# Kernel optimization log

Hardware: AMD Instinct MI355X
Metric: run time of the kernel (lower is better)

## Reference

```python
import jax, jax.numpy as jnp
import numpy as np

N, IN_FEAT, OUT_FEAT, H = 4096, 256, 256, 8
D = OUT_FEAT // H  # per-head dim = 32
ADJ_DENSITY = 0.05


def setup_inputs() -> dict:
    key = jax.random.key(0)
    kx, kw, kb, ka, kadj = jax.random.split(key, 5)
    x = jax.random.normal(kx, (N, IN_FEAT), dtype=jnp.float32)
    # eqx.nn.Linear params: weight [out, in], bias [out]
    W = jax.random.normal(kw, (OUT_FEAT, IN_FEAT), dtype=jnp.float32) * (1.0 / np.sqrt(IN_FEAT))
    b = jax.random.normal(kb, (OUT_FEAT,), dtype=jnp.float32) * 0.01
    a = jax.random.normal(ka, (H, 2 * D), dtype=jnp.float32)
    adj_matrix = jax.random.bernoulli(kadj, ADJ_DENSITY, (N, N)).astype(jnp.float32)
    return {"x": x, "W": W, "b": b, "a": a, "adj_matrix": adj_matrix}


def reference(x, W, b, a, adj_matrix):
    num_nodes = x.shape[0]
    num_heads = a.shape[0]
    half = a.shape[1] // 2
    # projection: [N, H*D] -> [N, H, D]
    node_feats = (x @ W.T + b).reshape(num_nodes, num_heads, half)
    # per-head additive attention halves -> [N, H]
    logit_parent = (node_feats * a[None, :, :half]).sum(axis=-1)
    logit_child = (node_feats * a[None, :, half:]).sum(axis=-1)
    # [N, N, H] dense logits via broadcast-add
    attn_logits = logit_parent[:, None, :] + logit_child[None, :, :]
    attn_logits = jax.nn.leaky_relu(attn_logits, 0.2)
    # NOTE: faithful to source — masked entries set to 0.0 (not -inf)
    attn_logits = jnp.where(jnp.abs(adj_matrix)[..., None] != 0.0, attn_logits, 0.0)
    attn_probs = jax.nn.softmax(attn_logits, axis=1)
    out = jnp.einsum('ijh,jhc->ihc', attn_probs, node_feats)
    return out.reshape(num_nodes, -1)
```

## Files before the change

kernel.cpp:

```cpp
#include <hip/hip_runtime.h>

#define NN    4096
#define OF    256
#define NH    8
#define MAXNZ 384

typedef __attribute__((ext_vector_type(8))) short short8;
typedef __attribute__((ext_vector_type(4))) float f32x4;

__device__ __forceinline__ float bf2f(unsigned int u) {
    union { unsigned int i; float f; } v; v.i = u << 16; return v.f;
}
__device__ __forceinline__ unsigned short f2bf(float f) {
    union { float f; unsigned int i; } v; v.f = f;
    unsigned int x = v.i;
    return (unsigned short)((x + 0x7fffu + ((x >> 16) & 1u)) >> 16);
}
__device__ __forceinline__ unsigned int pk2bf(float a, float b) {
    return (unsigned int)f2bf(a) | ((unsigned int)f2bf(b) << 16);
}

__global__ __launch_bounds__(256) void k_proj(
    const void* __restrict__ xraw, const void* __restrict__ Wraw,
    const void* __restrict__ braw, const void* __restrict__ araw,
    const float* __restrict__ adjf,
    unsigned short* __restrict__ nfb, float* __restrict__ lp,
    float* __restrict__ lc, float* __restrict__ Stot, int* __restrict__ flag,
    unsigned short* __restrict__ csr, int* __restrict__ nnz)
{
    __shared__ int viol;
    int t = threadIdx.x;
    if (t == 0) viol = 0;
    __syncthreads();
    int bad = 0;
    for (int k = t; k < NN; k += 256) {
        float v = adjf[k];
        if (!(v == 0.0f || v == 1.0f)) bad = 1;
    }
    if (bad) atomicAdd(&viol, 1);
    __syncthreads();
    int f = viol > 0;
    if (t == 0 && blockIdx.x == 0) *flag = f;

    int wave = t >> 6;
    int lane = t & 63;
    int tid  = blockIdx.x * 4 + wave;
    int mt = tid >> 4, nt = tid & 15;
    int lr = lane & 15;
    int kq = (lane >> 4) * 8;

    f32x4 acc = {0.f, 0.f, 0.f, 0.f};
    if (f) {
        const short8* xp = reinterpret_cast<const short8*>(
            (const unsigned short*)xraw + (size_t)(mt*16 + lr)*OF + kq);
        const short8* wp = reinterpret_cast<const short8*>(
            (const unsigned short*)Wraw + (size_t)(nt*16 + lr)*OF + kq);
        #pragma unroll
        for (int kk = 0; kk < OF/32; kk++)
            acc = __builtin_amdgcn_mfma_f32_16x16x32_bf16(xp[kk*4], wp[kk*4], acc, 0, 0, 0);
    } else {
        const float* xp = (const float*)xraw + (size_t)(mt*16 + lr)*OF + kq;
        const float* wp = (const float*)Wraw + (size_t)(nt*16 + lr)*OF + kq;
        #pragma unroll
        for (int kk = 0; kk < OF/32; kk++) {
            short8 ah, al, bh, bl;
            #pragma unroll
            for (int e = 0; e < 8; e++) {
                float xv = xp[kk*32 + e];
                unsigned short h = f2bf(xv);
                ah[e] = (short)h; al[e] = (short)f2bf(xv - bf2f(h));
                float wv = wp[kk*32 + e];
                unsigned short g = f2bf(wv);
                bh[e] = (short)g; bl[e] = (short)f2bf(wv - bf2f(g));
            }
            acc = __builtin_amdgcn_mfma_f32_16x16x32_bf16(ah, bh, acc, 0, 0, 0);
            acc = __builtin_amdgcn_mfma_f32_16x16x32_bf16(ah, bl, acc, 0, 0, 0);
            acc = __builtin_amdgcn_mfma_f32_16x16x32_bf16(al, bh, acc, 0, 0, 0);
        }
    }

    int col  = nt*16 + lr;
    int row0 = mt*16 + (lane >> 4) * 4;
    int h = col >> 5, cc = col & 31;
    float bias, apar, achd;
    if (f) {
        bias = bf2f((unsigned int)((const unsigned short*)braw)[col]);
        apar = bf2f((unsigned int)((const unsigned short*)araw)[h*64 + cc]);
        achd = bf2f((unsigned int)((const unsigned short*)araw)[h*64 + 32 + cc]);
    } else {
        bias = ((const float*)braw)[col];
        apar = ((const float*)araw)[h*64 + cc];
        achd = ((const float*)araw)[h*64 + 32 + cc];
    }
    float st = 0.f, pr[4], cr[4];
    #pragma unroll
    for (int r = 0; r < 4; r++) {
        float v = acc[r] + bias;
        nfb[(size_t)(row0 + r) * OF + col] = f2bf(v);
        st += v;
        pr[r] = v * apar;
        cr[r] = v * achd;
    }
    #pragma unroll
    for (int m = 1; m <= 8; m <<= 1) {
        #pragma unroll
        for (int r = 0; r < 4; r++) {
            pr[r] += __shfl_xor(pr[r], m, 64);
            cr[r] += __shfl_xor(cr[r], m, 64);
        }
    }
    if ((lane & 15) == 0) {
        #pragma unroll
        for (int r = 0; r < 4; r++) {
            atomicAdd(&lp[(row0 + r) * NH + h], pr[r]);
            atomicAdd(&lc[(row0 + r) * NH + h], cr[r]);
        }
    }
    st += __shfl_down(st, 16, 64);
    st += __shfl_down(st, 32, 64);
    if (lane < 16) atomicAdd(&Stot[col], st);

    int r = tid;
    unsigned long long m64 = 0ULL;
    if (f) {
        const uint4* arow = reinterpret_cast<const uint4*>(
            (const unsigned short*)adjf + (size_t)r * NN);
        #pragma unroll
        for (int g = 0; g < 8; g++) {
            uint4 v = arow[lane + 64*g];
            unsigned int wd[4] = {v.x, v.y, v.z, v.w};
            #pragma unroll
            for (int u = 0; u < 4; u++) {
                if (wd[u] & 0xffffu) m64 |= 1ULL << (g*8 + 2*u);
                if (wd[u] >> 16)     m64 |= 1ULL << (g*8 + 2*u + 1);
            }
        }
    } else {
        const uint4* arow = reinterpret_cast<const uint4*>(adjf + (size_t)r * NN);
        #pragma unroll 8
        for (int g = 0; g < 16; g++) {
            uint4 v = arow[lane + 64*g];
            if (v.x) m64 |= 1ULL << (g*4);
            if (v.y) m64 |= 1ULL << (g*4 + 1);
            if (v.z) m64 |= 1ULL << (g*4 + 2);
            if (v.w) m64 |= 1ULL << (g*4 + 3);
        }
    }
    int pc = __popcll(m64);
    int pref = pc;
    #pragma unroll
    for (int off = 1; off < 64; off <<= 1) {
        int u = __shfl_up(pref, off, 64);
        if (lane >= off) pref += u;
    }
    if (lane == 63) nnz[r] = min(pref, MAXNZ);
    {
        int pos = pref - pc;
        unsigned long long mm = m64;
        while (mm && pos < MAXNZ) {
            int q = __builtin_ctzll(mm);
            mm &= mm - 1;
            int j = f ? (lane*8 + ((q >> 3) << 9) + (q & 7))
                      : (lane*4 + ((q >> 2) << 8) + (q & 3));
            csr[(size_t)r * MAXNZ + pos++] = (unsigned short)j;
        }
    }
}

__global__ __launch_bounds__(256, 8) void k_attn(
    const int* __restrict__ flag, const unsigned short* __restrict__ csr,
    const int* __restrict__ nnz,
    const float* __restrict__ lp, const float* __restrict__ lc,
    const unsigned short* __restrict__ nfb, const float* __restrict__ Stot,
    void* __restrict__ outv)
{
    __shared__ float lps[NH];
    __shared__ int   jro[MAXNZ];
    __shared__ float wlist[MAXNZ][NH];
    __shared__ float zred[256];
    __shared__ float gred[3][256];

    int i = blockIdx.x;
    int t = threadIdx.x;
    int lane = t & 63, wid = t >> 6;
    int f = *flag;
    if (t < NH) lps[t] = lp[i*NH + t];
    int n = min(nnz[i], MAXNZ);

    if (t < MAXNZ/8) {
        uint4 v = reinterpret_cast<const uint4*>(csr + (size_t)i * MAXNZ)[t];
        unsigned int ws[4] = {v.x, v.y, v.z, v.w};
        #pragma unroll
        for (int u = 0; u < 4; u++) {
            jro[t*8 + 2*u]     = (int)(ws[u] & 0xffffu) * OF;
            jro[t*8 + 2*u + 1] = (int)(ws[u] >> 16) * OF;
        }
    }
    __syncthreads();

    int h8 = t & 7, c32 = t >> 3;
    float lph = lps[h8];
    float zp = 0.f;
    int k3 = c32;
    for (; k3 + 32 < n; k3 += 64) {
        int j0 = jro[k3] >> 5, j1 = jro[k3 + 32] >> 5;
        float l0 = lc[j0 + h8], l1 = lc[j1 + h8];
        float s0 = lph + l0; s0 = s0 > 0.f ? s0 : 0.2f * s0;
        float s1 = lph + l1; s1 = s1 > 0.f ? s1 : 0.2f * s1;
        float w0 = __expf(fminf(s0, 70.f)) - 1.f;
        float w1 = __expf(fminf(s1, 70.f)) - 1.f;
        wlist[k3][h8] = w0; wlist[k3 + 32][h8] = w1;
        zp += w0 + w1;
    }
    if (k3 < n) {
        float s = lph + lc[(jro[k3] >> 5) + h8];
        s = s > 0.f ? s : 0.2f * s;
        float w = __expf(fminf(s, 70.f)) - 1.f;
        wlist[k3][h8] = w;
        zp += w;
    }
    zred[t] = zp;
    __syncthreads();

    int hh = lane >> 3;
    int c4 = lane * 4;
    float a0 = 0.f, a1 = 0.f, a2 = 0.f, a3 = 0.f;
    int k = wid;
    for (; k + 28 < n; k += 32) {
        int jj[8]; float ww[8];
        #pragma unroll
        for (int u = 0; u < 8; u++) {
            jj[u] = __builtin_amdgcn_readfirstlane(jro[k + 4*u]);
            ww[u] = wlist[k + 4*u][hh];
        }
        uint2 d[8];
        #pragma unroll
        for (int u = 0; u < 8; u++)
            d[u] = *reinterpret_cast<const uint2*>(nfb + jj[u] + c4);
        #pragma unroll
        for (int u = 0; u < 8; u++) {
            a0 += ww[u] * bf2f(d[u].x & 0xffffu);
            a1 += ww[u] * bf2f(d[u].x >> 16);
            a2 += ww[u] * bf2f(d[u].y & 0xffffu);
            a3 += ww[u] * bf2f(d[u].y >> 16);
        }
    }
    for (; k < n; k += 4) {
        int j = __builtin_amdgcn_readfirstlane(jro[k]);
        float w = wlist[k][hh];
        uint2 d = *reinterpret_cast<const uint2*>(nfb + j + c4);
        a0 += w * bf2f(d.x & 0xffffu);
        a1 += w * bf2f(d.x >> 16);
        a2 += w * bf2f(d.y & 0xffffu);
        a3 += w * bf2f(d.y >> 16);
    }
    if (wid) {
        gred[wid-1][c4]   = a0; gred[wid-1][c4+1] = a1;
        gred[wid-1][c4+2] = a2; gred[wid-1][c4+3] = a3;
    }
    __syncthreads();

    if (wid == 0) {
        float z = zred[lane] + zred[lane+64] + zred[lane+128] + zred[lane+192];
        z += __shfl_down(z, 32, 64);
        z += __shfl_down(z, 16, 64);
        z += __shfl_down(z, 8, 64);
        float zfull = __shfl(z, hh, 64);
        float iz = 1.0f / (4096.0f + zfull);
        a0 += gred[0][c4]   + gred[1][c4]   + gred[2][c4];
        a1 += gred[0][c4+1] + gred[1][c4+1] + gred[2][c4+1];
        a2 += gred[0][c4+2] + gred[1][c4+2] + gred[2][c4+2];
        a3 += gred[0][c4+3] + gred[1][c4+3] + gred[2][c4+3];
        float4 stv = *reinterpret_cast<const float4*>(Stot + c4);
        float o0 = (stv.x + a0) * iz;
        float o1 = (stv.y + a1) * iz;
        float o2 = (stv.z + a2) * iz;
        float o3 = (stv.w + a3) * iz;
        if (f) {
            uint2 pk; pk.x = pk2bf(o0, o1); pk.y = pk2bf(o2, o3);
            *reinterpret_cast<uint2*>((unsigned short*)outv + (size_t)i*OF + c4) = pk;
        } else {
            float4 o = {o0, o1, o2, o3};
            *reinterpret_cast<float4*>((float*)outv + (size_t)i*OF + c4) = o;
        }
    }
}

extern "C" void kernel_launch(void* const* d_in, const int* in_sizes, int n_in,
                              void* d_out, int out_size, void* d_ws, size_t ws_size,
                              hipStream_t stream) {
    const void* x   = d_in[0];
    const void* W   = d_in[1];
    const void* b   = d_in[2];
    const void* a   = d_in[3];
    const void* adj = d_in[4];

    char* ws = (char*)d_ws;
    const size_t MB = 1024u*1024u, KB = 1024u;
    unsigned short* nfb  = (unsigned short*)(ws);
    float*          lp   = (float*)(ws + 2*MB);
    float*          lc   = (float*)(ws + 2*MB + 128*KB);
    float*          Stot = (float*)(ws + 2*MB + 256*KB);
    int*            flag = (int*)(ws + 2*MB + 257*KB);
    unsigned short* csr  = (unsigned short*)(ws + 2*MB + 258*KB);
    int*            nnz  = (int*)(ws + 5*MB + 258*KB);

    hipMemsetAsync(lp, 0, 257*KB, stream);
    k_proj <<<1024, 256, 0, stream>>>(x, W, b, a, (const float*)adj,
                                      nfb, lp, lc, Stot, flag, csr, nnz);
    k_attn <<<NN,   256, 0, stream>>>(flag, csr, nnz, lp, lc, nfb, Stot, d_out);
}
```

Before: 156.5 us.

## Split preprocessing kernel: precompute bf16 hi/lo splits of x and W

Adds a k_pre kernel that does the adjacency-to-CSR compaction and, on the fp32 path, converts x and W once into bf16 high/low halves stored in workspace. k_proj then loads these pre-split short8 vectors directly instead of doing strided scalar fp32 loads and per-element conversion inside every MFMA tile, where each W element was converted redundantly by many waves. In exchange it adds an extra kernel launch, writes and reads about 8 MB of extra workspace traffic, and reads the flag from global memory.

```diff
diff --git a/kernel.cpp b/kernel.cpp
--- a/kernel.cpp
+++ b/kernel.cpp
@@ -20,13 +20,12 @@
     return (unsigned int)f2bf(a) | ((unsigned int)f2bf(b) << 16);
 }
 
-__global__ __launch_bounds__(256) void k_proj(
-    const void* __restrict__ xraw, const void* __restrict__ Wraw,
-    const void* __restrict__ braw, const void* __restrict__ araw,
-    const float* __restrict__ adjf,
-    unsigned short* __restrict__ nfb, float* __restrict__ lp,
-    float* __restrict__ lc, float* __restrict__ Stot, int* __restrict__ flag,
-    unsigned short* __restrict__ csr, int* __restrict__ nnz)
+__global__ __launch_bounds__(256) void k_pre(
+    const float* __restrict__ adjf, const float* __restrict__ xf,
+    const float* __restrict__ Wf, int* __restrict__ flag,
+    unsigned short* __restrict__ csr, int* __restrict__ nnz,
+    unsigned short* __restrict__ xbh, unsigned short* __restrict__ xbl,
+    unsigned short* __restrict__ Wbh, unsigned short* __restrict__ Wbl)
 {
     __shared__ int viol;
     int t = threadIdx.x;
@@ -42,6 +41,81 @@
     int f = viol > 0;
     if (t == 0 && blockIdx.x == 0) *flag = f;
 
+    int lane = t & 63, wid = t >> 6;
+    int r = blockIdx.x * 4 + wid;
+
+    unsigned long long m64 = 0ULL;
+    if (f) {
+        const uint4* arow = reinterpret_cast<const uint4*>(
+            (const unsigned short*)adjf + (size_t)r * NN);
+        #pragma unroll
+        for (int g = 0; g < 8; g++) {
+            uint4 v = arow[lane + 64*g];
+            unsigned int wd[4] = {v.x, v.y, v.z, v.w};
+            #pragma unroll
+            for (int u = 0; u < 4; u++) {
+                if (wd[u] & 0xffffu) m64 |= 1ULL << (g*8 + 2*u);
+                if (wd[u] >> 16)     m64 |= 1ULL << (g*8 + 2*u + 1);
+            }
+        }
+    } else {
+        const uint4* arow = reinterpret_cast<const uint4*>(adjf + (size_t)r * NN);
+        #pragma unroll 8
+        for (int g = 0; g < 16; g++) {
+            uint4 v = arow[lane + 64*g];
+            if (v.x) m64 |= 1ULL << (g*4);
+            if (v.y) m64 |= 1ULL << (g*4 + 1);
+            if (v.z) m64 |= 1ULL << (g*4 + 2);
+            if (v.w) m64 |= 1ULL << (g*4 + 3);
+        }
+    }
+    int pc = __popcll(m64);
+    int pref = pc;
+    #pragma unroll
+    for (int off = 1; off < 64; off <<= 1) {
+        int u = __shfl_up(pref, off, 64);
+        if (lane >= off) pref += u;
+    }
+    if (lane == 63) nnz[r] = min(pref, MAXNZ);
+    {
+        int pos = pref - pc;
+        unsigned long long mm = m64;
+        while (mm && pos < MAXNZ) {
+            int q = __builtin_ctzll(mm);
+            mm &= mm - 1;
+            int j = f ? (lane*8 + ((q >> 3) << 9) + (q & 7))
+                      : (lane*4 + ((q >> 2) << 8) + (q & 3));
+            csr[(size_t)r * MAXNZ + pos++] = (unsigned short)j;
+        }
+    }
+
+    if (!f) {
+        const int NX = NN * OF, NTOT = NX + OF * OF;
+        for (int e = blockIdx.x * 256 + t; e < NTOT; e += 1024 * 256) {
+            if (e < NX) {
+                float v = xf[e];
+                unsigned short h = f2bf(v);
+                xbh[e] = h; xbl[e] = f2bf(v - bf2f(h));
+            } else {
+                float v = Wf[e - NX];
+                unsigned short h = f2bf(v);
+                Wbh[e - NX] = h; Wbl[e - NX] = f2bf(v - bf2f(h));
+            }
+        }
+    }
+}
+
+__global__ __launch_bounds__(256) void k_proj(
+    const void* __restrict__ xraw, const void* __restrict__ Wraw,
+    const void* __restrict__ braw, const void* __restrict__ araw,
+    const int* __restrict__ flag,
+    const unsigned short* __restrict__ xbh, const unsigned short* __restrict__ xbl,
+    const unsigned short* __restrict__ Wbh, const unsigned short* __restrict__ Wbl,
+    unsigned short* __restrict__ nfb, float* __restrict__ lp,
+    float* __restrict__ lc, float* __restrict__ Stot)
+{
+    int f = *flag;
+    int t = threadIdx.x;
     int wave = t >> 6;
     int lane = t & 63;
     int tid  = blockIdx.x * 4 + wave;
@@ -49,30 +123,25 @@
     int lr = lane & 15;
     int kq = (lane >> 4) * 8;
 
+    size_t xo = (size_t)(mt*16 + lr)*OF + kq;
+    size_t wo = (size_t)(nt*16 + lr)*OF + kq;
+
     f32x4 acc = {0.f, 0.f, 0.f, 0.f};
     if (f) {
-        const short8* xp = reinterpret_cast<const short8*>(
-            (const unsigned short*)xraw + (size_t)(mt*16 + lr)*OF + kq);
-        const short8* wp = reinterpret_cast<const short8*>(
-            (const unsigned short*)Wraw + (size_t)(nt*16 + lr)*OF + kq);
+        const short8* xp = reinterpret_cast<const short8*>((const unsigned short*)xraw + xo);
+        const short8* wp = reinterpret_cast<const short8*>((const unsigned short*)Wraw + wo);
         #pragma unroll
         for (int kk = 0; kk < OF/32; kk++)
             acc = __builtin_amdgcn_mfma_f32_16x16x32_bf16(xp[kk*4], wp[kk*4], acc, 0, 0, 0);
     } else {
-        const float* xp = (const float*)xraw + (size_t)(mt*16 + lr)*OF + kq;
-        const float* wp = (const float*)Wraw + (size_t)(nt*16 + lr)*OF + kq;
+        const short8* xh = reinterpret_cast<const short8*>(xbh + xo);
+        const short8* xl = reinterpret_cast<const short8*>(xbl + xo);
+        const short8* wh = reinterpret_cast<const short8*>(Wbh + wo);
+        const short8* wl = reinterpret_cast<const short8*>(Wbl + wo);
         #pragma unroll
         for (int kk = 0; kk < OF/32; kk++) {
-            short8 ah, al, bh, bl;
-            #pragma unroll
-            for (int e = 0; e < 8; e++) {
-                float xv = xp[kk*32 + e];
-                unsigned short h = f2bf(xv);
-                ah[e] = (short)h; al[e] = (short)f2bf(xv - bf2f(h));
-                float wv = wp[kk*32 + e];
-                unsigned short g = f2bf(wv);
-                bh[e] = (short)g; bl[e] = (short)f2bf(wv - bf2f(g));
-            }
+            short8 ah = xh[kk*4], al = xl[kk*4];
+            short8 bh = wh[kk*4], bl = wl[kk*4];
             acc = __builtin_amdgcn_mfma_f32_16x16x32_bf16(ah, bh, acc, 0, 0, 0);
             acc = __builtin_amdgcn_mfma_f32_16x16x32_bf16(ah, bl, acc, 0, 0, 0);
             acc = __builtin_amdgcn_mfma_f32_16x16x32_bf16(al, bh, acc, 0, 0, 0);
@@ -119,52 +188,6 @@
     st += __shfl_down(st, 16, 64);
     st += __shfl_down(st, 32, 64);
     if (lane < 16) atomicAdd(&Stot[col], st);
-
-    int r = tid;
-    unsigned long long m64 = 0ULL;
-    if (f) {
-        const uint4* arow = reinterpret_cast<const uint4*>(
-            (const unsigned short*)adjf + (size_t)r * NN);
-        #pragma unroll
-        for (int g = 0; g < 8; g++) {
-            uint4 v = arow[lane + 64*g];
-            unsigned int wd[4] = {v.x, v.y, v.z, v.w};
-            #pragma unroll
-            for (int u = 0; u < 4; u++) {
-                if (wd[u] & 0xffffu) m64 |= 1ULL << (g*8 + 2*u);
-                if (wd[u] >> 16)     m64 |= 1ULL << (g*8 + 2*u + 1);
-            }
-        }
-    } else {
-        const uint4* arow = reinterpret_cast<const uint4*>(adjf + (size_t)r * NN);
-        #pragma unroll 8
-        for (int g = 0; g < 16; g++) {
-            uint4 v = arow[lane + 64*g];
-            if (v.x) m64 |= 1ULL << (g*4);
-            if (v.y) m64 |= 1ULL << (g*4 + 1);
-            if (v.z) m64 |= 1ULL << (g*4 + 2);
-            if (v.w) m64 |= 1ULL << (g*4 + 3);
-        }
-    }
-    int pc = __popcll(m64);
-    int pref = pc;
-    #pragma unroll
-    for (int off = 1; off < 64; off <<= 1) {
-        int u = __shfl_up(pref, off, 64);
-        if (lane >= off) pref += u;
-    }
-    if (lane == 63) nnz[r] = min(pref, MAXNZ);
-    {
-        int pos = pref - pc;
-        unsigned long long mm = m64;
-        while (mm && pos < MAXNZ) {
-            int q = __builtin_ctzll(mm);
-            mm &= mm - 1;
-            int j = f ? (lane*8 + ((q >> 3) << 9) + (q & 7))
-                      : (lane*4 + ((q >> 2) << 8) + (q & 3));
-            csr[(size_t)r * MAXNZ + pos++] = (unsigned short)j;
-        }
-    }
 }
 
 __global__ __launch_bounds__(256, 8) void k_attn(
@@ -304,9 +327,16 @@
     int*            flag = (int*)(ws + 2*MB + 257*KB);
     unsigned short* csr  = (unsigned short*)(ws + 2*MB + 258*KB);
     int*            nnz  = (int*)(ws + 5*MB + 258*KB);
+    unsigned short* xbh  = (unsigned short*)(ws + 6*MB);
+    unsigned short* xbl  = (unsigned short*)(ws + 8*MB);
+    unsigned short* Wbh  = (unsigned short*)(ws + 10*MB);
+    unsigned short* Wbl  = (unsigned short*)(ws + 10*MB + 128*KB);
 
     hipMemsetAsync(lp, 0, 257*KB, stream);
-    k_proj <<<1024, 256, 0, stream>>>(x, W, b, a, (const float*)adj,
-                                      nfb, lp, lc, Stot, flag, csr, nnz);
+    k_pre  <<<1024, 256, 0, stream>>>((const float*)adj, (const float*)x,
+                                      (const float*)W, flag, csr, nnz,
+                                      xbh, xbl, Wbh, Wbl);
+    k_proj <<<1024, 256, 0, stream>>>(x, W, b, a, flag, xbh, xbl, Wbh, Wbl,
+                                      nfb, lp, lc, Stot);
     k_attn <<<NN,   256, 0, stream>>>(flag, csr, nnz, lp, lc, nfb, Stot, d_out);
 }
```

After: 173.0 us. 10.5% more time.

## Precompute bf16 hi/lo split of W in a pre-kernel and stage x tiles in LDS

Applied to the files above, without the earlier changes.

Adds a k_pre kernel that runs the adjacency-format check, zeroes the lp/lc/Stot workspace in place of hipMemsetAsync, and converts W once into bf16 high and low halves. k_proj then loads the pre-split W directly and converts each 16-row x tile into LDS once per block instead of per-lane strided scalar loads. This removes redundant fp32-to-bf16 split work and uncoalesced global loads in the projection, at the cost of an extra kernel launch and 17 KB of LDS per block.

```diff
diff --git a/kernel.cpp b/kernel.cpp
--- a/kernel.cpp
+++ b/kernel.cpp
@@ -20,16 +20,14 @@
     return (unsigned int)f2bf(a) | ((unsigned int)f2bf(b) << 16);
 }
 
-__global__ __launch_bounds__(256) void k_proj(
-    const void* __restrict__ xraw, const void* __restrict__ Wraw,
-    const void* __restrict__ braw, const void* __restrict__ araw,
-    const float* __restrict__ adjf,
-    unsigned short* __restrict__ nfb, float* __restrict__ lp,
-    float* __restrict__ lc, float* __restrict__ Stot, int* __restrict__ flag,
-    unsigned short* __restrict__ csr, int* __restrict__ nnz)
+__global__ __launch_bounds__(256) void k_pre(
+    const float* __restrict__ adjf, const float* __restrict__ Wf,
+    int* __restrict__ flag, unsigned short* __restrict__ Wbh,
+    unsigned short* __restrict__ Wbl, float* __restrict__ zbase)
 {
     __shared__ int viol;
     int t = threadIdx.x;
+    int gid = blockIdx.x * 256 + t;
     if (t == 0) viol = 0;
     __syncthreads();
     int bad = 0;
@@ -40,8 +38,30 @@
     if (bad) atomicAdd(&viol, 1);
     __syncthreads();
     int f = viol > 0;
-    if (t == 0 && blockIdx.x == 0) *flag = f;
-
+    if (t == 0) *flag = f;
+
+    zbase[gid] = 0.f;
+    if (gid < 256) zbase[65536 + gid] = 0.f;
+    if (!f) {
+        float v = Wf[gid];
+        unsigned short h = f2bf(v);
+        Wbh[gid] = h; Wbl[gid] = f2bf(v - bf2f(h));
+    }
+}
+
+__global__ __launch_bounds__(256) void k_proj(
+    const void* __restrict__ xraw, const void* __restrict__ Wraw,
+    const void* __restrict__ braw, const void* __restrict__ araw,
+    const float* __restrict__ adjf, const int* __restrict__ flag,
+    const unsigned short* __restrict__ Wbh, const unsigned short* __restrict__ Wbl,
+    unsigned short* __restrict__ nfb, float* __restrict__ lp,
+    float* __restrict__ lc, float* __restrict__ Stot,
+    unsigned short* __restrict__ csr, int* __restrict__ nnz)
+{
+    __shared__ unsigned short xh[16][264], xl[16][264];
+
+    int f = *flag;
+    int t = threadIdx.x;
     int wave = t >> 6;
     int lane = t & 63;
     int tid  = blockIdx.x * 4 + wave;
@@ -49,30 +69,37 @@
     int lr = lane & 15;
     int kq = (lane >> 4) * 8;
 
+    if (!f) {
+        const float* xsrc = (const float*)xraw + (size_t)mt * 4096;
+        #pragma unroll
+        for (int q = 0; q < 16; q++) {
+            int e = t + 256*q;
+            float v = xsrc[e];
+            unsigned short h = f2bf(v);
+            xh[e >> 8][e & 255] = h;
+            xl[e >> 8][e & 255] = f2bf(v - bf2f(h));
+        }
+        __syncthreads();
+    }
+
+    size_t wo = (size_t)(nt*16 + lr)*OF + kq;
     f32x4 acc = {0.f, 0.f, 0.f, 0.f};
     if (f) {
         const short8* xp = reinterpret_cast<const short8*>(
             (const unsigned short*)xraw + (size_t)(mt*16 + lr)*OF + kq);
         const short8* wp = reinterpret_cast<const short8*>(
-            (const unsigned short*)Wraw + (size_t)(nt*16 + lr)*OF + kq);
+            (const unsigned short*)Wraw + wo);
         #pragma unroll
         for (int kk = 0; kk < OF/32; kk++)
             acc = __builtin_amdgcn_mfma_f32_16x16x32_bf16(xp[kk*4], wp[kk*4], acc, 0, 0, 0);
     } else {
-        const float* xp = (const float*)xraw + (size_t)(mt*16 + lr)*OF + kq;
-        const float* wp = (const float*)Wraw + (size_t)(nt*16 + lr)*OF + kq;
+        const short8* wh = reinterpret_cast<const short8*>(Wbh + wo);
+        const short8* wl = reinterpret_cast<const short8*>(Wbl + wo);
         #pragma unroll
         for (int kk = 0; kk < OF/32; kk++) {
-            short8 ah, al, bh, bl;
-            #pragma unroll
-            for (int e = 0; e < 8; e++) {
-                float xv = xp[kk*32 + e];
-                unsigned short h = f2bf(xv);
-                ah[e] = (short)h; al[e] = (short)f2bf(xv - bf2f(h));
-                float wv = wp[kk*32 + e];
-                unsigned short g = f2bf(wv);
-                bh[e] = (short)g; bl[e] = (short)f2bf(wv - bf2f(g));
-            }
+            short8 ah = *reinterpret_cast<const short8*>(&xh[lr][kk*32 + kq]);
+            short8 al = *reinterpret_cast<const short8*>(&xl[lr][kk*32 + kq]);
+            short8 bh = wh[kk*4], bl = wl[kk*4];
             acc = __builtin_amdgcn_mfma_f32_16x16x32_bf16(ah, bh, acc, 0, 0, 0);
             acc = __builtin_amdgcn_mfma_f32_16x16x32_bf16(ah, bl, acc, 0, 0, 0);
             acc = __builtin_amdgcn_mfma_f32_16x16x32_bf16(al, bh, acc, 0, 0, 0);
@@ -304,9 +331,12 @@
     int*            flag = (int*)(ws + 2*MB + 257*KB);
     unsigned short* csr  = (unsigned short*)(ws + 2*MB + 258*KB);
     int*            nnz  = (int*)(ws + 5*MB + 258*KB);
-
-    hipMemsetAsync(lp, 0, 257*KB, stream);
-    k_proj <<<1024, 256, 0, stream>>>(x, W, b, a, (const float*)adj,
-                                      nfb, lp, lc, Stot, flag, csr, nnz);
+    unsigned short* Wbh  = (unsigned short*)(ws + 6*MB);
+    unsigned short* Wbl  = (unsigned short*)(ws + 6*MB + 128*KB);
+
+    k_pre  <<<256,  256, 0, stream>>>((const float*)adj, (const float*)W,
+                                      flag, Wbh, Wbl, lp);
+    k_proj <<<1024, 256, 0, stream>>>(x, W, b, a, (const float*)adj, flag,
+                                      Wbh, Wbl, nfb, lp, lc, Stot, csr, nnz);
     k_attn <<<NN,   256, 0, stream>>>(flag, csr, nnz, lp, lc, nfb, Stot, d_out);
 }
```

Result: no change. 159.1 us (+1.7%).
